# Optimization experiments

Hardware: AMD Instinct MI355X
Metric: run time of the kernel (lower is better)

## Reference

```python
import jax, jax.numpy as jnp
import numpy as np

TEMPERATURE = 0.5

def setup_inputs() -> dict:
    key = jax.random.key(0)
    k1, k2 = jax.random.split(key)
    B, D = 4096, 128
    emb_i = jax.random.normal(k1, (B, D), dtype=jnp.float32)
    emb_j = jax.random.normal(k2, (B, D), dtype=jnp.float32)
    return {"emb_i": emb_i, "emb_j": emb_j}

def reference(emb_i, emb_j):
    B = emb_i.shape[0]
    # L2 normalize each view (F.normalize, dim=1)
    z_i = emb_i / jnp.linalg.norm(emb_i, axis=1, keepdims=True)
    z_j = emb_j / jnp.linalg.norm(emb_j, axis=1, keepdims=True)
    reps = jnp.concatenate([z_i, z_j], axis=0)  # [2B, D], unit rows
    # cosine similarity of unit vectors == dot product (use GEMM, not broadcast)
    sim = reps @ reps.T  # [2B, 2B]
    # positives: sim[k, k+B] for k<B and sim[k+B, k] for k<B
    idx = jnp.arange(B)
    sim_ij = sim[idx, idx + B]
    sim_ji = sim[idx + B, idx]
    positives = jnp.concatenate([sim_ij, sim_ji], axis=0)  # [2B]
    nominator = jnp.exp(positives / TEMPERATURE)
    # mask out self-similarity diagonal in the denominator
    neg_mask = 1.0 - jnp.eye(2 * B, dtype=sim.dtype)
    denominator = jnp.sum(neg_mask * jnp.exp(sim / TEMPERATURE), axis=1)  # [2B]
    loss_partial = -jnp.log(nominator / denominator)
    loss = jnp.sum(loss_partial) / (2 * B)
    return loss
```

## Files before the change

kernel.cpp:

```cpp
#include <hip/hip_runtime.h>
#include <hip/hip_bf16.h>
#include <math.h>

typedef __attribute__((ext_vector_type(8))) short bf16x8;
typedef __attribute__((ext_vector_type(4))) float f32x4;
typedef __attribute__((ext_vector_type(2))) float f32x2;

constexpr int B_ = 4096;
constexpr int N_ = 8192;
constexpr int D_ = 128;
constexpr float INV_T = 2.0f;
constexpr float EXP2C = 2.0f * 1.4426950408889634f;
constexpr float E2C = 7.38905609893065f;


__global__ __launch_bounds__(256) void nrm_kernel(const float* __restrict__ ei,
                                                  const float* __restrict__ ej,
                                                  short* __restrict__ zf,
                                                  float* __restrict__ pos,
                                                  float* __restrict__ out) {
    int p    = (blockIdx.x * blockDim.x + threadIdx.x) >> 6;
    int lane = threadIdx.x & 63;
    if (p >= B_) return;
    f32x2 a = *(const f32x2*)(ei + (size_t)p * D_ + lane * 2);
    f32x2 b = *(const f32x2*)(ej + (size_t)p * D_ + lane * 2);
    float na = a.x * a.x + a.y * a.y;
    float nb = b.x * b.x + b.y * b.y;
    float dt = a.x * b.x + a.y * b.y;
    #pragma unroll
    for (int m = 1; m < 64; m <<= 1) {
        na += __shfl_xor(na, m);
        nb += __shfl_xor(nb, m);
        dt += __shfl_xor(dt, m);
    }
    float ra = rsqrtf(na), rb = rsqrtf(nb);
    __hip_bfloat162 oa, ob;
    oa.x = __float2bfloat16(a.x * ra); oa.y = __float2bfloat16(a.y * ra);
    ob.x = __float2bfloat16(b.x * rb); ob.y = __float2bfloat16(b.y * rb);
    size_t fi = (size_t)(lane >> 2) * 128 + (p & 15) * 8 + (lane & 3) * 2;
    *(__hip_bfloat162*)(zf + (size_t)(p >> 4) * 2048 + fi)          = oa;
    *(__hip_bfloat162*)(zf + (size_t)((p + B_) >> 4) * 2048 + fi)   = ob;
    if (lane == 0) {
        pos[p] = dt * ra * rb;
        if (p == 0) out[0] = 0.0f;
    }
}

constexpr int NJ = 32;
constexpr int BLK_ROWS = 256;
constexpr int JCHUNK = N_ / NJ;
constexpr int NT = JCHUNK / 16;

__global__ __launch_bounds__(256) void simsum_kernel(const short* __restrict__ zf,
                                                     float* __restrict__ part) {
    int lane = threadIdx.x & 63;
    int wave = threadIdx.x >> 6;
    int r0   = blockIdx.x * BLK_ROWS + wave * 64;
    int pr0  = r0 >> 4;
    int pj0  = (blockIdx.y * JCHUNK) >> 4;
    int g  = lane >> 4;
    int lm = lane & 15;

    const short* ZA = zf + (size_t)pr0 * 2048 + lane * 8;
    const short* ZB = zf + (size_t)pj0 * 2048 + lane * 8;

    bf16x8 a[4][4];
    #pragma unroll
    for (int t = 0; t < 4; ++t)
        #pragma unroll
        for (int s = 0; s < 4; ++s)
            a[t][s] = *(const bf16x8*)(ZA + t * 2048 + s * 512);

    f32x4 rs[4];
    #pragma unroll
    for (int t = 0; t < 4; ++t) rs[t] = f32x4{0.f, 0.f, 0.f, 0.f};

    bf16x8 b[3][4];
    #pragma unroll
    for (int s = 0; s < 4; ++s) b[0][s] = *(const bf16x8*)(ZB + 0 * 2048 + s * 512);
    #pragma unroll
    for (int s = 0; s < 4; ++s) b[1][s] = *(const bf16x8*)(ZB + 1 * 2048 + s * 512);

    #pragma unroll
    for (int jt = 0; jt < NT; ++jt) {
        if (jt + 2 < NT) {
            #pragma unroll
            for (int s = 0; s < 4; ++s)
                b[(jt + 2) % 3][s] = *(const bf16x8*)(ZB + (size_t)(jt + 2) * 2048 + s * 512);
        }
        f32x4 acc[4];
        #pragma unroll
        for (int t = 0; t < 4; ++t) acc[t] = f32x4{0.f, 0.f, 0.f, 0.f};
        #pragma unroll
        for (int s = 0; s < 4; ++s)
            #pragma unroll
            for (int t = 0; t < 4; ++t)
                acc[t] = __builtin_amdgcn_mfma_f32_16x16x32_bf16(a[t][s], b[jt % 3][s], acc[t], 0, 0, 0);
        #pragma unroll
        for (int t = 0; t < 4; ++t)
            #pragma unroll
            for (int r = 0; r < 4; ++r)
                rs[t][r] += exp2f(EXP2C * acc[t][r]);
    }

    #pragma unroll
    for (int m = 1; m < 16; m <<= 1)
        #pragma unroll
        for (int t = 0; t < 4; ++t)
            #pragma unroll
            for (int r = 0; r < 4; ++r)
                rs[t][r] += __shfl_xor(rs[t][r], m);

    if (lm == 0) {
        float* pr = part + (size_t)blockIdx.y * N_ + r0;
        #pragma unroll
        for (int t = 0; t < 4; ++t)
            #pragma unroll
            for (int r = 0; r < 4; ++r)
                pr[t * 16 + g * 4 + r] = rs[t][r];
    }
}

__global__ __launch_bounds__(256) void loss_kernel(const float* __restrict__ part,
                                                   const float* __restrict__ pos,
                                                   float* __restrict__ out) {
    int tid = threadIdx.x;
    int k   = blockIdx.x * 256 + tid;
    float d = 0.0f;
    #pragma unroll
    for (int c = 0; c < NJ; ++c) d += part[(size_t)c * N_ + k];
    d -= E2C;
    float v = __logf(d) - pos[k & (B_ - 1)] * INV_T;
    #pragma unroll
    for (int m = 1; m < 64; m <<= 1) v += __shfl_xor(v, m);
    __shared__ float ps[4];
    if ((tid & 63) == 0) ps[tid >> 6] = v;
    __syncthreads();
    if (tid == 0)
        atomicAdd(out, (ps[0] + ps[1] + ps[2] + ps[3]) * (1.0f / N_));
}

extern "C" void kernel_launch(void* const* d_in, const int* in_sizes, int n_in,
                              void* d_out, int out_size, void* d_ws, size_t ws_size,
                              hipStream_t stream) {
    const float* ei = (const float*)d_in[0];
    const float* ej = (const float*)d_in[1];
    float* out = (float*)d_out;

    short* zf   = (short*)d_ws;
    float* pos  = (float*)((char*)d_ws + (size_t)N_ * D_ * 2);
    float* part = pos + B_;

    nrm_kernel<<<dim3(B_ / 4), dim3(256), 0, stream>>>(ei, ej, zf, pos, out);
    simsum_kernel<<<dim3(N_ / BLK_ROWS, NJ), dim3(256), 0, stream>>>(zf, part);
    loss_kernel<<<dim3(N_ / 256), dim3(256), 0, stream>>>(part, pos, out);
}
```

Before: 97.00 us.

## Exploit symmetry of similarity matrix by computing only upper-triangular tiles

The similarity GEMM now covers only upper-triangular 128x128 tiles of the symmetric 8192x8192 matrix. Each tile adds its exp-sums to both the row partials and, through LDS, the column partials of the mirrored tile, so the partial buffer grows to 64 slices per row. This roughly halves the MFMA and exp work. In exchange it adds a serial loop to decode the triangular block index, an extra cross-lane reduction per panel, an LDS barrier, and a larger partial-sum read in the loss kernel.

Measured after the change: 99.62 us. +2.7%, slower.

```diff
diff --git a/kernel.cpp b/kernel.cpp
--- a/kernel.cpp
+++ b/kernel.cpp
@@ -12,6 +12,11 @@
 constexpr float INV_T = 2.0f;
 constexpr float EXP2C = 2.0f * 1.4426950408889634f;
 constexpr float E2C = 7.38905609893065f;
+
+constexpr int TILE = 128;
+constexpr int NTI  = N_ / TILE;
+constexpr int NBLK = NTI * (NTI + 1) / 2;
+constexpr int NPAN = TILE / 16;
 
 
 __global__ __launch_bounds__(256) void nrm_kernel(const float* __restrict__ ei,
@@ -38,31 +43,27 @@
     oa.x = __float2bfloat16(a.x * ra); oa.y = __float2bfloat16(a.y * ra);
     ob.x = __float2bfloat16(b.x * rb); ob.y = __float2bfloat16(b.y * rb);
     size_t fi = (size_t)(lane >> 2) * 128 + (p & 15) * 8 + (lane & 3) * 2;
-    *(__hip_bfloat162*)(zf + (size_t)(p >> 4) * 2048 + fi)          = oa;
-    *(__hip_bfloat162*)(zf + (size_t)((p + B_) >> 4) * 2048 + fi)   = ob;
+    *(__hip_bfloat162*)(zf + (size_t)(p >> 4) * 2048 + fi)        = oa;
+    *(__hip_bfloat162*)(zf + (size_t)((p + B_) >> 4) * 2048 + fi) = ob;
     if (lane == 0) {
         pos[p] = dt * ra * rb;
         if (p == 0) out[0] = 0.0f;
     }
 }
 
-constexpr int NJ = 32;
-constexpr int BLK_ROWS = 256;
-constexpr int JCHUNK = N_ / NJ;
-constexpr int NT = JCHUNK / 16;
-
-__global__ __launch_bounds__(256) void simsum_kernel(const short* __restrict__ zf,
+__global__ __launch_bounds__(128) void simsum_kernel(const short* __restrict__ zf,
                                                      float* __restrict__ part) {
     int lane = threadIdx.x & 63;
     int wave = threadIdx.x >> 6;
-    int r0   = blockIdx.x * BLK_ROWS + wave * 64;
-    int pr0  = r0 >> 4;
-    int pj0  = (blockIdx.y * JCHUNK) >> 4;
+    int bi = 0, rem = blockIdx.x;
+    while (rem >= NTI - bi) { rem -= NTI - bi; ++bi; }
+    int bj = bi + rem;
+
     int g  = lane >> 4;
     int lm = lane & 15;
 
-    const short* ZA = zf + (size_t)pr0 * 2048 + lane * 8;
-    const short* ZB = zf + (size_t)pj0 * 2048 + lane * 8;
+    const short* ZA = zf + (size_t)(bi * 8 + wave * 4) * 2048 + lane * 8;
+    const short* ZB = zf + (size_t)(bj * 8) * 2048 + lane * 8;
 
     bf16x8 a[4][4];
     #pragma unroll
@@ -74,6 +75,7 @@
     f32x4 rs[4];
     #pragma unroll
     for (int t = 0; t < 4; ++t) rs[t] = f32x4{0.f, 0.f, 0.f, 0.f};
+    float cs[NPAN];
 
     bf16x8 b[3][4];
     #pragma unroll
@@ -82,8 +84,8 @@
     for (int s = 0; s < 4; ++s) b[1][s] = *(const bf16x8*)(ZB + 1 * 2048 + s * 512);
 
     #pragma unroll
-    for (int jt = 0; jt < NT; ++jt) {
-        if (jt + 2 < NT) {
+    for (int jt = 0; jt < NPAN; ++jt) {
+        if (jt + 2 < NPAN) {
             #pragma unroll
             for (int s = 0; s < 4; ++s)
                 b[(jt + 2) % 3][s] = *(const bf16x8*)(ZB + (size_t)(jt + 2) * 2048 + s * 512);
@@ -96,11 +98,18 @@
             #pragma unroll
             for (int t = 0; t < 4; ++t)
                 acc[t] = __builtin_amdgcn_mfma_f32_16x16x32_bf16(a[t][s], b[jt % 3][s], acc[t], 0, 0, 0);
+        float ca = 0.f;
         #pragma unroll
         for (int t = 0; t < 4; ++t)
             #pragma unroll
-            for (int r = 0; r < 4; ++r)
-                rs[t][r] += exp2f(EXP2C * acc[t][r]);
+            for (int r = 0; r < 4; ++r) {
+                float e = exp2f(EXP2C * acc[t][r]);
+                rs[t][r] += e;
+                ca += e;
+            }
+        ca += __shfl_xor(ca, 16);
+        ca += __shfl_xor(ca, 32);
+        cs[jt] = ca;
     }
 
     #pragma unroll
@@ -112,12 +121,25 @@
                 rs[t][r] += __shfl_xor(rs[t][r], m);
 
     if (lm == 0) {
-        float* pr = part + (size_t)blockIdx.y * N_ + r0;
+        float* pr = part + (size_t)bj * N_ + bi * TILE + wave * 64;
         #pragma unroll
         for (int t = 0; t < 4; ++t)
             #pragma unroll
             for (int r = 0; r < 4; ++r)
                 pr[t * 16 + g * 4 + r] = rs[t][r];
+    }
+
+    __shared__ float lds[2 * TILE];
+    if (lane < 16) {
+        #pragma unroll
+        for (int jt = 0; jt < NPAN; ++jt)
+            lds[wave * TILE + jt * 16 + lane] = cs[jt];
+    }
+    __syncthreads();
+    if (bi != bj) {
+        int tid = threadIdx.x;
+        float v = lds[tid] + lds[TILE + tid];
+        part[(size_t)bi * N_ + bj * TILE + tid] = v;
     }
 }
 
@@ -128,7 +150,7 @@
     int k   = blockIdx.x * 256 + tid;
     float d = 0.0f;
     #pragma unroll
-    for (int c = 0; c < NJ; ++c) d += part[(size_t)c * N_ + k];
+    for (int c = 0; c < NTI; ++c) d += part[(size_t)c * N_ + k];
     d -= E2C;
     float v = __logf(d) - pos[k & (B_ - 1)] * INV_T;
     #pragma unroll
@@ -152,6 +174,6 @@
     float* part = pos + B_;
 
     nrm_kernel<<<dim3(B_ / 4), dim3(256), 0, stream>>>(ei, ej, zf, pos, out);
-    simsum_kernel<<<dim3(N_ / BLK_ROWS, NJ), dim3(256), 0, stream>>>(zf, part);
+    simsum_kernel<<<dim3(NBLK), dim3(128), 0, stream>>>(zf, part);
     loss_kernel<<<dim3(N_ / 256), dim3(256), 0, stream>>>(part, pos, out);
 }
```
